# Kernel tuning notes

Hardware: AMD Instinct MI355X
Metric: run time of the kernel (lower is better)

## Reference

```python
import jax, jax.numpy as jnp
import numpy as np

DEGREE = 8


def _askey_wilson_basis(x, a, b, c, d, q, degree):
    # Iterative 3-term recurrence (same math as the recursive torch version).
    # x: (batch, input_dim); a,b,c,d,q: scalars broadcast over x.
    basis = [jnp.ones_like(x)]
    if degree >= 1:
        p1 = (2 * (1 + a * b * q) * x - (a + b) * (1 + c * d * q)) / (1 + a * b * c * d * q ** 2)
        basis.append(p1)
    for n in range(2, degree + 1):
        An = (1 - a * b * q ** (n - 1)) * (1 - c * d * q ** (n - 1)) * (1 - a * b * c * d * q ** (2 * n - 2))
        An = An / ((1 - a * b * c * d * q ** (2 * n - 1)) * (1 - a * b * c * d * q ** (2 * n)))
        Cn = (1 - q ** n) * (1 - a * b * q ** (n - 1)) * (1 - c * d * q ** (n - 1)) * (1 - a * b * c * d * q ** (2 * n - 2))
        Cn = Cn / ((1 - a * b * c * d * q ** (2 * n - 2)) * (1 - a * b * c * d * q ** (2 * n - 1)))
        pn = ((2 * x - An) * basis[n - 1] - Cn * basis[n - 2]) / (1 - q ** n)
        basis.append(pn)
    return jnp.stack(basis, axis=-1)  # (batch, input_dim, degree+1)


def setup_inputs() -> dict:
    key = jax.random.key(0)
    k1, k2, k3, k4, k5, k6, k7 = jax.random.split(key, 7)
    input_dim, output_dim, degree = 1024, 1024, DEGREE
    batch = 8192
    x = jax.random.normal(k1, (batch, input_dim), dtype=jnp.float32)
    a = jax.random.normal(k2, (1,), dtype=jnp.float32)
    b = jax.random.normal(k3, (1,), dtype=jnp.float32)
    c = jax.random.normal(k4, (1,), dtype=jnp.float32)
    d = jax.random.normal(k5, (1,), dtype=jnp.float32)
    q = jax.random.normal(k6, (1,), dtype=jnp.float32)
    std = 1.0 / (input_dim * (degree + 1))
    coeffs = jax.random.normal(k7, (input_dim, output_dim, degree + 1), dtype=jnp.float32) * std
    return {"x": x, "a": a, "b": b, "c": c, "d": d, "q": q, "coeffs": coeffs}


def reference(x, a, b, c, d, q, coeffs) -> jnp.ndarray:
    a0, b0, c0, d0, q0 = a[0], b[0], c[0], d[0], q[0]
    basis = _askey_wilson_basis(x, a0, b0, c0, d0, q0, DEGREE)  # (b, i, d+1)
    y = jnp.einsum('bid,iod->bo', basis, coeffs)
    return y
```

## Files before the change

kernel.cpp:

```cpp
#include <hip/hip_runtime.h>
#include <cstdint>

typedef unsigned short u16;
typedef __bf16 bf16x8 __attribute__((ext_vector_type(8)));
typedef float f32x4 __attribute__((ext_vector_type(4)));

#define M_DIM 8192
#define N_DIM 1024
#define I_DIM 1024
#define NDEG 8
#define K_DIM (I_DIM * NDEG)
#define BM 256
#define BN 128
#define BK 64
#define NT (K_DIM / BK)
#define A_TILE (BM * BK)
#define B_TILE (BN * BK)

__device__ __forceinline__ u16 f2bf(float f) {
    union { float f; uint32_t u; } v; v.f = f;
    return (u16)((v.u + 0x7FFFu + ((v.u >> 16) & 1u)) >> 16);
}

__device__ __forceinline__ void gload_lds16(const u16* g, u16* l) {
    auto lp = reinterpret_cast<__attribute__((address_space(3))) uint32_t*>(
        reinterpret_cast<uintptr_t>(l));
    __builtin_amdgcn_global_load_lds(reinterpret_cast<const uint32_t*>(g), lp, 16, 0, 0);
}

__device__ __forceinline__ void do_transform_block(
    int blk, int t, const float* __restrict__ coeffs,
    u16* __restrict__ Bt, float* __restrict__ bias, float (*lds)[292])
{
    int bi = blk >> 5, bo = blk & 31;
    int i0 = bi * 32, o0 = bo * 32;

    {
        int r = t >> 3, s = t & 7;
        const float4* src = (const float4*)(coeffs + ((size_t)(i0 + r) * N_DIM + o0) * 9);
#pragma unroll
        for (int j = 0; j < 9; ++j) {
            float4 v = src[s * 9 + j];
            *(float4*)&lds[r][(s * 9 + j) * 4] = v;
        }
    }
    __syncthreads();

    {
        int c = t >> 3, s2 = t & 7;
        u16 ob[32];
#pragma unroll
        for (int rr = 0; rr < 4; ++rr)
#pragma unroll
            for (int dd = 0; dd < 8; ++dd)
                ob[rr * 8 + dd] = f2bf(lds[s2 * 4 + rr][c * 9 + 1 + dd]);
        uint4* dst = (uint4*)(Bt + (size_t)(o0 + c) * K_DIM + (size_t)i0 * 8 + s2 * 32);
        const uint4* sp = (const uint4*)ob;
#pragma unroll
        for (int u = 0; u < 4; ++u) dst[u] = sp[u];
    }

    if (t < 32) {
        float sum = 0.f;
#pragma unroll
        for (int rr = 0; rr < 32; ++rr) sum += lds[rr][t * 9];
        atomicAdd(&bias[o0 + t], sum);
    }
}

__device__ __forceinline__ void do_basis_thread(
    int gt, const float* __restrict__ x,
    const float* __restrict__ pa, const float* __restrict__ pb,
    const float* __restrict__ pc, const float* __restrict__ pd,
    const float* __restrict__ pq, u16* __restrict__ A, int row0)
{
    int rb = gt >> 7;
    int g  = gt & 127;
    int i0 = g << 3;
    int b  = row0 + rb;

    float a = *pa, bb = *pb, c = *pc, d = *pd, q = *pq;
    float ab = a * bb, cd = c * d, abcd = ab * cd;

    float qp[17];
    qp[0] = 1.f;
#pragma unroll
    for (int k = 1; k <= 16; ++k) qp[k] = qp[k - 1] * q;

    float den1 = 1.f + abcd * q * q;
    float c1x = 2.f * (1.f + ab * q) / den1;
    float c1c = -(a + bb) * (1.f + cd * q) / den1;

    float An[9], Cn[9], Sn[9];
#pragma unroll
    for (int n = 2; n <= 8; ++n) {
        float t1 = 1.f - ab * qp[n - 1];
        float t2 = 1.f - cd * qp[n - 1];
        float t3 = 1.f - abcd * qp[2 * n - 2];
        float t4 = 1.f - abcd * qp[2 * n - 1];
        float t5 = 1.f - abcd * qp[2 * n];
        An[n] = (t1 * t2 * t3) / (t4 * t5);
        Cn[n] = ((1.f - qp[n]) * t1 * t2 * t3) / (t3 * t4);
        Sn[n] = 1.f / (1.f - qp[n]);
    }

    const float4* x4 = (const float4*)(x + (size_t)b * I_DIM + i0);
    float4 v0 = x4[0], v1 = x4[1];
    float xv[8] = {v0.x, v0.y, v0.z, v0.w, v1.x, v1.y, v1.z, v1.w};

    u16 ob[64];
#pragma unroll
    for (int j = 0; j < 8; ++j) {
        float xj = xv[j];
        float p1 = c1x * xj + c1c;
        ob[j * 8 + 0] = f2bf(p1);
        float pm2 = 1.f, pm1 = p1;
#pragma unroll
        for (int n = 2; n <= 8; ++n) {
            float pn = ((2.f * xj - An[n]) * pm1 - Cn[n] * pm2) * Sn[n];
            ob[j * 8 + n - 1] = f2bf(pn);
            pm2 = pm1; pm1 = pn;
        }
    }

    uint4* dst = (uint4*)(A + (size_t)rb * K_DIM + (size_t)i0 * 8);
    const uint4* s = (const uint4*)ob;
#pragma unroll
    for (int u = 0; u < 8; ++u) dst[u] = s[u];
}

__global__ __launch_bounds__(256) void aw_prep(
    const float* __restrict__ coeffs, const float* __restrict__ x,
    const float* __restrict__ pa, const float* __restrict__ pb,
    const float* __restrict__ pc, const float* __restrict__ pd,
    const float* __restrict__ pq,
    u16* __restrict__ Bt, float* __restrict__ bias, u16* __restrict__ A)
{
    __shared__ float lds[32][292];
    int blk = blockIdx.x;
    int t = threadIdx.x;
    if (blk < 1024) {
        do_transform_block(blk, t, coeffs, Bt, bias, lds);
    } else {
        int gt = (blk - 1024) * 256 + t;
        do_basis_thread(gt, x, pa, pb, pc, pd, pq, A, 0);
    }
}

__global__ __launch_bounds__(256) void aw_transform(
    const float* __restrict__ coeffs, u16* __restrict__ Bt, float* __restrict__ bias)
{
    __shared__ float lds[32][292];
    do_transform_block(blockIdx.x, threadIdx.x, coeffs, Bt, bias, lds);
}

__global__ void aw_basis(const float* __restrict__ x,
                         const float* __restrict__ pa, const float* __restrict__ pb,
                         const float* __restrict__ pc, const float* __restrict__ pd,
                         const float* __restrict__ pq,
                         u16* __restrict__ A, int row0)
{
    do_basis_thread(blockIdx.x * 256 + threadIdx.x, x, pa, pb, pc, pd, pq, A, row0);
}

__global__ __launch_bounds__(512) void aw_gemm(
    const u16* __restrict__ A,
    const u16* __restrict__ B,
    const float* __restrict__ bias,
    float* __restrict__ C,
    int row0, int rowBlocks)
{
    __shared__ alignas(16) u16 smem[3 * A_TILE + 3 * B_TILE];
    u16* As = smem;
    u16* Bs = smem + 3 * A_TILE;

    int nwg = rowBlocks * 8;
    int bid = blockIdx.x;
    int per = nwg >> 3;
    int logical = (bid & 7) * per + (bid >> 3);
    int rowBlk = logical >> 3;
    int colBlk = logical & 7;

    const int tid  = threadIdx.x;
    const int lane = tid & 63;
    const int wid  = tid >> 6;
    const int quad = wid & 3;
    const int wr   = quad >> 1;
    const int wc   = quad & 1;
    const int myKs = wid >> 2;

    const u16* gA[4]; const u16* gB[2];
    int ldsA[4], ldsB[2];
#pragma unroll
    for (int j = 0; j < 4; ++j) {
        int idx = j * 512 + tid;
        int r = idx >> 3, sl = idx & 7;
        gA[j] = A + (size_t)rowBlk * BM * K_DIM + (size_t)r * K_DIM + ((sl ^ (r & 7)) << 3);
        ldsA[j] = idx << 3;
    }
#pragma unroll
    for (int j = 0; j < 2; ++j) {
        int idx = j * 512 + tid;
        int r = idx >> 3, sl = idx & 7;
        gB[j] = B + (size_t)colBlk * BN * K_DIM + (size_t)r * K_DIM + ((sl ^ (r & 7)) << 3);
        ldsB[j] = idx << 3;
    }

    int offA[8], offB[4];
#pragma unroll
    for (int mi = 0; mi < 8; ++mi) {
        int r = wr * 128 + mi * 16 + (lane & 15);
        int s = myKs * 4 + (lane >> 4);
        offA[mi] = r * 128 + ((s ^ (r & 7)) << 4);
    }
#pragma unroll
    for (int ni = 0; ni < 4; ++ni) {
        int r = wc * 64 + ni * 16 + (lane & 15);
        int s = myKs * 4 + (lane >> 4);
        offB[ni] = r * 128 + ((s ^ (r & 7)) << 4);
    }

    f32x4 acc[8][4];
#pragma unroll
    for (int mi = 0; mi < 8; ++mi)
#pragma unroll
        for (int ni = 0; ni < 4; ++ni)
            acc[mi][ni] = (f32x4){0.f, 0.f, 0.f, 0.f};

    auto stage = [&](int kt, int buf) {
        const int k0 = kt * BK;
        u16* dA = As + buf * A_TILE;
        u16* dB = Bs + buf * B_TILE;
        gload_lds16(gA[0] + k0, dA + ldsA[0]);
        gload_lds16(gA[1] + k0, dA + ldsA[1]);
        gload_lds16(gA[2] + k0, dA + ldsA[2]);
        gload_lds16(gA[3] + k0, dA + ldsA[3]);
        gload_lds16(gB[0] + k0, dB + ldsB[0]);
        gload_lds16(gB[1] + k0, dB + ldsB[1]);
    };

    stage(0, 0);
    stage(1, 1);
    asm volatile("s_waitcnt vmcnt(6)" ::: "memory");
    __builtin_amdgcn_s_barrier();

    int buf = 0;
    for (int t = 0; t < NT; ++t) {
        const char* aB = (const char*)(As + buf * A_TILE);
        const char* bB = (const char*)(Bs + buf * B_TILE);
        int nb = buf + 2; if (nb >= 3) nb -= 3;
        const bool pf = (t + 2 < NT);

        bf16x8 fa[8], fb[4];
#pragma unroll
        for (int mi = 0; mi < 4; ++mi) fa[mi] = *(const bf16x8*)(aB + offA[mi]);
#pragma unroll
        for (int ni = 0; ni < 2; ++ni) fb[ni] = *(const bf16x8*)(bB + offB[ni]);
        if (pf) stage(t + 2, nb);
#pragma unroll
        for (int mi = 4; mi < 8; ++mi) fa[mi] = *(const bf16x8*)(aB + offA[mi]);
#pragma unroll
        for (int ni = 2; ni < 4; ++ni) fb[ni] = *(const bf16x8*)(bB + offB[ni]);

        __builtin_amdgcn_s_setprio(1);
#pragma unroll
        for (int mi = 0; mi < 8; ++mi)
#pragma unroll
            for (int ni = 0; ni < 4; ++ni)
                acc[mi][ni] = __builtin_amdgcn_mfma_f32_16x16x32_bf16(
                    fa[mi], fb[ni], acc[mi][ni], 0, 0, 0);
        __builtin_amdgcn_s_setprio(0);

        if (pf)              { asm volatile("s_waitcnt vmcnt(6)" ::: "memory"); }
        else if (t + 1 < NT) { asm volatile("s_waitcnt vmcnt(0)" ::: "memory"); }
        __builtin_amdgcn_s_barrier();

        buf += 1; if (buf >= 3) buf -= 3;
    }

    float* red = (float*)smem;
    if (myKs == 1) {
        f32x4* dst = (f32x4*)red + quad * 2048;
#pragma unroll
        for (int mi = 0; mi < 8; ++mi)
#pragma unroll
            for (int ni = 0; ni < 4; ++ni)
                dst[(mi * 4 + ni) * 64 + lane] = acc[mi][ni];
    }
    __syncthreads();
    if (myKs == 0) {
        const f32x4* src = (const f32x4*)red + quad * 2048;
#pragma unroll
        for (int mi = 0; mi < 8; ++mi)
#pragma unroll
            for (int ni = 0; ni < 4; ++ni) {
                f32x4 p = src[(mi * 4 + ni) * 64 + lane];
                acc[mi][ni] += p;
            }

        int gRow = row0 + rowBlk * BM + wr * 128;
        int gCol = colBlk * BN + wc * 64;
#pragma unroll
        for (int mi = 0; mi < 8; ++mi) {
#pragma unroll
            for (int ni = 0; ni < 4; ++ni) {
                int rr = gRow + mi * 16 + ((lane >> 4) << 2);
                int cc = gCol + ni * 16 + (lane & 15);
                float bv = bias[cc];
                float* dst = C + (size_t)rr * N_DIM + cc;
#pragma unroll
                for (int j = 0; j < 4; ++j) dst[(size_t)j * N_DIM] = acc[mi][ni][j] + bv;
            }
        }
    }
}

extern "C" void kernel_launch(void* const* d_in, const int* in_sizes, int n_in,
                              void* d_out, int out_size, void* d_ws, size_t ws_size,
                              hipStream_t stream)
{
    const float* x      = (const float*)d_in[0];
    const float* pa     = (const float*)d_in[1];
    const float* pb     = (const float*)d_in[2];
    const float* pc     = (const float*)d_in[3];
    const float* pd     = (const float*)d_in[4];
    const float* pq     = (const float*)d_in[5];
    const float* coeffs = (const float*)d_in[6];
    float* out = (float*)d_out;

    float* bias = (float*)d_ws;
    const size_t biasBytes = 4096;
    u16* Bt = (u16*)((char*)d_ws + biasBytes);
    const size_t btBytes = (size_t)N_DIM * K_DIM * sizeof(u16);
    u16* Abuf = (u16*)((char*)d_ws + biasBytes + btBytes);
    size_t used = biasBytes + btBytes;
    size_t avail = ws_size > used ? ws_size - used : 0;
    const size_t aFullBytes = (size_t)M_DIM * K_DIM * sizeof(u16);

    hipMemsetAsync(bias, 0, N_DIM * sizeof(float), stream);

    if (avail >= aFullBytes) {
        aw_prep<<<1024 + (M_DIM * 128) / 256, 256, 0, stream>>>(
            coeffs, x, pa, pb, pc, pd, pq, Bt, bias, Abuf);
        aw_gemm<<<(M_DIM / BM) * 8, 512, 0, stream>>>(Abuf, Bt, bias, out, 0, M_DIM / BM);
    } else {
        int chunk = M_DIM;
        while (chunk > 256 && (size_t)chunk * K_DIM * sizeof(u16) > avail) chunk >>= 1;
        aw_transform<<<1024, 256, 0, stream>>>(coeffs, Bt, bias);
        for (int row0 = 0; row0 < M_DIM; row0 += chunk) {
            aw_basis<<<(chunk * 128) / 256, 256, 0, stream>>>(x, pa, pb, pc, pd, pq, Abuf, row0);
            aw_gemm<<<(chunk / BM) * 8, 512, 0, stream>>>(Abuf, Bt, bias, out, row0, chunk / BM);
        }
    }
}
```

Measured before the change: 181.4 us.

## Ping-pong wave groups between MFMA and LDS fragment loads per K tile

Replaces the split-K-within-tile scheme, where each wave group handled half of every BK slice, with a ping-pong schedule. The two wave groups alternate whole K tiles: one runs MFMAs on its preloaded fragments while the other waits for the global loads and reads the next tile's fragments from LDS. The prefetch distance also grows from two tiles ahead to three. This aims to overlap LDS reads with matrix math across waves, at the cost of doubling fragment registers (fa/fb now [..][2]) and possibly lowering occupancy or causing spills.

```diff
diff --git a/kernel.cpp b/kernel.cpp
--- a/kernel.cpp
+++ b/kernel.cpp
@@ -187,7 +187,7 @@
     const int quad = wid & 3;
     const int wr   = quad >> 1;
     const int wc   = quad & 1;
-    const int myKs = wid >> 2;
+    const int grp  = wid >> 2;
 
     const u16* gA[4]; const u16* gB[2];
     int ldsA[4], ldsB[2];
@@ -206,19 +206,23 @@
         ldsB[j] = idx << 3;
     }
 
-    int offA[8], offB[4];
-#pragma unroll
-    for (int mi = 0; mi < 8; ++mi) {
-        int r = wr * 128 + mi * 16 + (lane & 15);
-        int s = myKs * 4 + (lane >> 4);
-        offA[mi] = r * 128 + ((s ^ (r & 7)) << 4);
-    }
-#pragma unroll
-    for (int ni = 0; ni < 4; ++ni) {
-        int r = wc * 64 + ni * 16 + (lane & 15);
-        int s = myKs * 4 + (lane >> 4);
-        offB[ni] = r * 128 + ((s ^ (r & 7)) << 4);
-    }
+    int offA[8][2], offB[4][2];
+#pragma unroll
+    for (int mi = 0; mi < 8; ++mi)
+#pragma unroll
+        for (int ks = 0; ks < 2; ++ks) {
+            int r = wr * 128 + mi * 16 + (lane & 15);
+            int s = ks * 4 + (lane >> 4);
+            offA[mi][ks] = r * 128 + ((s ^ (r & 7)) << 4);
+        }
+#pragma unroll
+    for (int ni = 0; ni < 4; ++ni)
+#pragma unroll
+        for (int ks = 0; ks < 2; ++ks) {
+            int r = wc * 64 + ni * 16 + (lane & 15);
+            int s = ks * 4 + (lane >> 4);
+            offB[ni][ks] = r * 128 + ((s ^ (r & 7)) << 4);
+        }
 
     f32x4 acc[8][4];
 #pragma unroll
@@ -239,47 +243,64 @@
         gload_lds16(gB[1] + k0, dB + ldsB[1]);
     };
 
+    bf16x8 fa[8][2], fb[4][2];
+
+    auto rdfrags = [&](int buf) {
+        const char* aB = (const char*)(As + buf * A_TILE);
+        const char* bB = (const char*)(Bs + buf * B_TILE);
+#pragma unroll
+        for (int mi = 0; mi < 8; ++mi) {
+            fa[mi][0] = *(const bf16x8*)(aB + offA[mi][0]);
+            fa[mi][1] = *(const bf16x8*)(aB + offA[mi][1]);
+        }
+#pragma unroll
+        for (int ni = 0; ni < 4; ++ni) {
+            fb[ni][0] = *(const bf16x8*)(bB + offB[ni][0]);
+            fb[ni][1] = *(const bf16x8*)(bB + offB[ni][1]);
+        }
+    };
+
     stage(0, 0);
     stage(1, 1);
-    asm volatile("s_waitcnt vmcnt(6)" ::: "memory");
+    stage(2, 2);
+    asm volatile("s_waitcnt vmcnt(12)" ::: "memory");
+    __builtin_amdgcn_s_barrier();
+    if (grp == 0) {
+        rdfrags(0);
+        asm volatile("s_waitcnt lgkmcnt(0)" ::: "memory");
+    }
     __builtin_amdgcn_s_barrier();
 
     int buf = 0;
     for (int t = 0; t < NT; ++t) {
-        const char* aB = (const char*)(As + buf * A_TILE);
-        const char* bB = (const char*)(Bs + buf * B_TILE);
-        int nb = buf + 2; if (nb >= 3) nb -= 3;
-        const bool pf = (t + 2 < NT);
-
-        bf16x8 fa[8], fb[4];
-#pragma unroll
-        for (int mi = 0; mi < 4; ++mi) fa[mi] = *(const bf16x8*)(aB + offA[mi]);
-#pragma unroll
-        for (int ni = 0; ni < 2; ++ni) fb[ni] = *(const bf16x8*)(bB + offB[ni]);
-        if (pf) stage(t + 2, nb);
-#pragma unroll
-        for (int mi = 4; mi < 8; ++mi) fa[mi] = *(const bf16x8*)(aB + offA[mi]);
-#pragma unroll
-        for (int ni = 2; ni < 4; ++ni) fb[ni] = *(const bf16x8*)(bB + offB[ni]);
-
-        __builtin_amdgcn_s_setprio(1);
-#pragma unroll
-        for (int mi = 0; mi < 8; ++mi)
-#pragma unroll
-            for (int ni = 0; ni < 4; ++ni)
-                acc[mi][ni] = __builtin_amdgcn_mfma_f32_16x16x32_bf16(
-                    fa[mi], fb[ni], acc[mi][ni], 0, 0, 0);
-        __builtin_amdgcn_s_setprio(0);
-
-        if (pf)              { asm volatile("s_waitcnt vmcnt(6)" ::: "memory"); }
-        else if (t + 1 < NT) { asm volatile("s_waitcnt vmcnt(0)" ::: "memory"); }
+        if (t + 3 < NT) stage(t + 3, buf);
+
+        if (((t & 1)) == grp) {
+            __builtin_amdgcn_s_setprio(1);
+#pragma unroll
+            for (int ks = 0; ks < 2; ++ks)
+#pragma unroll
+                for (int mi = 0; mi < 8; ++mi)
+#pragma unroll
+                    for (int ni = 0; ni < 4; ++ni)
+                        acc[mi][ni] = __builtin_amdgcn_mfma_f32_16x16x32_bf16(
+                            fa[mi][ks], fb[ni][ks], acc[mi][ni], 0, 0, 0);
+            __builtin_amdgcn_s_setprio(0);
+        } else if (t + 1 < NT) {
+            if (t + 3 < NT)      { asm volatile("s_waitcnt vmcnt(12)" ::: "memory"); }
+            else if (t + 2 < NT) { asm volatile("s_waitcnt vmcnt(6)"  ::: "memory"); }
+            else                 { asm volatile("s_waitcnt vmcnt(0)"  ::: "memory"); }
+            int nb = buf + 1; if (nb >= 3) nb -= 3;
+            rdfrags(nb);
+            asm volatile("s_waitcnt lgkmcnt(0)" ::: "memory");
+        }
+
         __builtin_amdgcn_s_barrier();
-
         buf += 1; if (buf >= 3) buf -= 3;
     }
 
     float* red = (float*)smem;
-    if (myKs == 1) {
+    if (grp == 1) {
         f32x4* dst = (f32x4*)red + quad * 2048;
 #pragma unroll
         for (int mi = 0; mi < 8; ++mi)
@@ -288,7 +309,7 @@
                 dst[(mi * 4 + ni) * 64 + lane] = acc[mi][ni];
     }
     __syncthreads();
-    if (myKs == 0) {
+    if (grp == 0) {
         const f32x4* src = (const f32x4*)red + quad * 2048;
 #pragma unroll
         for (int mi = 0; mi < 8; ++mi)
```

Result: slower. 199.5 us (+10.0%).

## Load GEMM A fragments directly from global into registers, bypassing LDS

Applied to the files above, without the earlier changes.

The A operand is no longer staged through LDS. Each wave loads its own bf16 A fragments straight from global memory into a register double buffer, one k-tile ahead, while B keeps the three-stage LDS pipeline. The aim is to remove LDS traffic and LDS capacity for A and to allow a single workgroup per CU. The cost is that waves sharing the same A rows each fetch them separately, so A global/L2 traffic doubles. The loads also touch only 64 contiguous bytes per row, which weakens coalescing and adds global-load latency that must be hidden before the MFMAs.

```diff
diff --git a/kernel.cpp b/kernel.cpp
--- a/kernel.cpp
+++ b/kernel.cpp
@@ -14,7 +14,6 @@
 #define BN 128
 #define BK 64
 #define NT (K_DIM / BK)
-#define A_TILE (BM * BK)
 #define B_TILE (BN * BK)
 
 __device__ __forceinline__ u16 f2bf(float f) {
@@ -163,16 +162,15 @@
     do_basis_thread(blockIdx.x * 256 + threadIdx.x, x, pa, pb, pc, pd, pq, A, row0);
 }
 
-__global__ __launch_bounds__(512) void aw_gemm(
+__global__ __launch_bounds__(512, 1) void aw_gemm(
     const u16* __restrict__ A,
     const u16* __restrict__ B,
     const float* __restrict__ bias,
     float* __restrict__ C,
     int row0, int rowBlocks)
 {
-    __shared__ alignas(16) u16 smem[3 * A_TILE + 3 * B_TILE];
-    u16* As = smem;
-    u16* Bs = smem + 3 * A_TILE;
+    __shared__ alignas(16) unsigned char smemraw[131072];
+    u16* Bs = (u16*)smemraw;
 
     int nwg = rowBlocks * 8;
     int bid = blockIdx.x;
@@ -189,15 +187,12 @@
     const int wc   = quad & 1;
     const int myKs = wid >> 2;
 
-    const u16* gA[4]; const u16* gB[2];
-    int ldsA[4], ldsB[2];
-#pragma unroll
-    for (int j = 0; j < 4; ++j) {
-        int idx = j * 512 + tid;
-        int r = idx >> 3, sl = idx & 7;
-        gA[j] = A + (size_t)rowBlk * BM * K_DIM + (size_t)r * K_DIM + ((sl ^ (r & 7)) << 3);
-        ldsA[j] = idx << 3;
-    }
+    const int aRow  = rowBlk * BM + wr * 128 + (lane & 15);
+    const int aSlot = myKs * 4 + (lane >> 4);
+    const u16* aF0 = A + (size_t)aRow * K_DIM + aSlot * 8;
+
+    const u16* gB[2];
+    int ldsB[2];
 #pragma unroll
     for (int j = 0; j < 2; ++j) {
         int idx = j * 512 + tid;
@@ -206,13 +201,7 @@
         ldsB[j] = idx << 3;
     }
 
-    int offA[8], offB[4];
-#pragma unroll
-    for (int mi = 0; mi < 8; ++mi) {
-        int r = wr * 128 + mi * 16 + (lane & 15);
-        int s = myKs * 4 + (lane >> 4);
-        offA[mi] = r * 128 + ((s ^ (r & 7)) << 4);
-    }
+    int offB[4];
 #pragma unroll
     for (int ni = 0; ni < 4; ++ni) {
         int r = wc * 64 + ni * 16 + (lane & 15);
@@ -227,41 +216,23 @@
         for (int ni = 0; ni < 4; ++ni)
             acc[mi][ni] = (f32x4){0.f, 0.f, 0.f, 0.f};
 
-    auto stage = [&](int kt, int buf) {
+    auto stageB = [&](int kt, int buf) {
         const int k0 = kt * BK;
-        u16* dA = As + buf * A_TILE;
         u16* dB = Bs + buf * B_TILE;
-        gload_lds16(gA[0] + k0, dA + ldsA[0]);
-        gload_lds16(gA[1] + k0, dA + ldsA[1]);
-        gload_lds16(gA[2] + k0, dA + ldsA[2]);
-        gload_lds16(gA[3] + k0, dA + ldsA[3]);
         gload_lds16(gB[0] + k0, dB + ldsB[0]);
         gload_lds16(gB[1] + k0, dB + ldsB[1]);
     };
-
-    stage(0, 0);
-    stage(1, 1);
-    asm volatile("s_waitcnt vmcnt(6)" ::: "memory");
-    __builtin_amdgcn_s_barrier();
-
-    int buf = 0;
-    for (int t = 0; t < NT; ++t) {
-        const char* aB = (const char*)(As + buf * A_TILE);
+    auto loadA = [&](bf16x8 (&fa)[8], int kt) {
+        const u16* p = aF0 + (size_t)kt * BK;
+#pragma unroll
+        for (int mi = 0; mi < 8; ++mi)
+            fa[mi] = *(const bf16x8*)(p + (size_t)mi * (16 * K_DIM));
+    };
+    auto domfma = [&](bf16x8 (&fa)[8], int buf) {
         const char* bB = (const char*)(Bs + buf * B_TILE);
-        int nb = buf + 2; if (nb >= 3) nb -= 3;
-        const bool pf = (t + 2 < NT);
-
-        bf16x8 fa[8], fb[4];
-#pragma unroll
-        for (int mi = 0; mi < 4; ++mi) fa[mi] = *(const bf16x8*)(aB + offA[mi]);
-#pragma unroll
-        for (int ni = 0; ni < 2; ++ni) fb[ni] = *(const bf16x8*)(bB + offB[ni]);
-        if (pf) stage(t + 2, nb);
-#pragma unroll
-        for (int mi = 4; mi < 8; ++mi) fa[mi] = *(const bf16x8*)(aB + offA[mi]);
-#pragma unroll
-        for (int ni = 2; ni < 4; ++ni) fb[ni] = *(const bf16x8*)(bB + offB[ni]);
-
+        bf16x8 fb[4];
+#pragma unroll
+        for (int ni = 0; ni < 4; ++ni) fb[ni] = *(const bf16x8*)(bB + offB[ni]);
         __builtin_amdgcn_s_setprio(1);
 #pragma unroll
         for (int mi = 0; mi < 8; ++mi)
@@ -270,15 +241,37 @@
                 acc[mi][ni] = __builtin_amdgcn_mfma_f32_16x16x32_bf16(
                     fa[mi], fb[ni], acc[mi][ni], 0, 0, 0);
         __builtin_amdgcn_s_setprio(0);
-
-        if (pf)              { asm volatile("s_waitcnt vmcnt(6)" ::: "memory"); }
-        else if (t + 1 < NT) { asm volatile("s_waitcnt vmcnt(0)" ::: "memory"); }
-        __builtin_amdgcn_s_barrier();
-
-        buf += 1; if (buf >= 3) buf -= 3;
-    }
-
-    float* red = (float*)smem;
+    };
+
+#define TILE_IT(T, CUR, NXT)                                                  \
+    do {                                                                      \
+        int b2 = buf + 2; if (b2 >= 3) b2 -= 3;                               \
+        if ((T) + 2 < NT) stageB((T) + 2, b2);                                \
+        if ((T) + 1 < NT) loadA(NXT, (T) + 1);                                \
+        domfma(CUR, buf);                                                     \
+        if ((T) + 1 < NT) {                                                   \
+            asm volatile("s_waitcnt vmcnt(8)" ::: "memory");                  \
+            __builtin_amdgcn_s_barrier();                                     \
+        }                                                                     \
+        buf += 1; if (buf >= 3) buf -= 3;                                     \
+    } while (0)
+
+    stageB(0, 0);
+    stageB(1, 1);
+    bf16x8 pa[8], qa[8];
+    loadA(pa, 0);
+    asm volatile("s_waitcnt vmcnt(8)" ::: "memory");
+    __builtin_amdgcn_s_barrier();
+
+    int buf = 0;
+    for (int t = 0; t < NT; t += 2) {
+        TILE_IT(t,     pa, qa);
+        TILE_IT(t + 1, qa, pa);
+    }
+#undef TILE_IT
+
+    __syncthreads();
+    float* red = (float*)smemraw;
     if (myKs == 1) {
         f32x4* dst = (f32x4*)red + quad * 2048;
 #pragma unroll
```

After: 338.3 us. 86.5% more time.
